# Kernel optimization log

Hardware: AMD Instinct MI355X
Metric: run time of the kernel (lower is better)

## Reference

```python
import jax, jax.numpy as jnp
import numpy as np

K = 2            # negative:positive edge ratio (init arg k)
N_NODES = 4096
N_EDGES = 8192
FEAT = 64


def setup_inputs() -> dict:
    key = jax.random.key(0)
    k1, k2, k3 = jax.random.split(key, 3)
    node_feature = jax.random.normal(k1, (N_NODES, FEAT), dtype=jnp.float32)
    edge_src = jax.random.randint(k2, (N_EDGES,), 0, N_NODES, dtype=jnp.int32)
    edge_dst = jax.random.randint(k3, (N_EDGES,), 0, N_NODES, dtype=jnp.int32)
    return {"node_feature": node_feature, "edge_src": edge_src, "edge_dst": edge_dst}


def reference(node_feature, edge_src, edge_dst):
    E = edge_src.shape[0]
    N = node_feature.shape[0]
    # [E, E] pairwise mask: candidate column j is valid for row i iff
    # dst[j] != dst[i] and dst[j] != src[i]
    valid = (edge_dst[:, None] != edge_dst[None, :]) & (edge_src[:, None] != edge_dst[None, :])
    # unsorted_segment_min over rows grouped by edge_src -> [N, E]
    segmin = jax.ops.segment_min(valid.astype(jnp.int8), edge_src, num_segments=N)
    # gather back per edge -> [E, E], flatten
    m = segmin[edge_src].reshape(-1).astype(bool)  # [E*E]
    num_negatives = jnp.sum(m)
    ratio = num_negatives // E                      # integer ratio as in TF code
    keep_prob = (K / ratio).astype(jnp.float32)
    u = jax.random.uniform(jax.random.key(42), (E * E,), dtype=jnp.float32)
    keep = m & (u < keep_prob)
    # fixed-size (jit-friendly) stand-in for tf.boolean_mask: expected count is K*E;
    # pad/truncate to exactly K*E kept flat indices (fill_value=0 pads).
    idx = jnp.nonzero(keep, size=K * E, fill_value=0)[0]
    rows = idx // E
    cols = idx % E
    edge_src_neg = edge_src[rows]
    edge_dst_neg = edge_dst[cols]
    return edge_src_neg, edge_dst_neg
```

## Files before the change

kernel.cpp:

```cpp
#include <hip/hip_runtime.h>
#include <stdint.h>
#include <math.h>

typedef unsigned int u32;
typedef unsigned long long u64;

#define E_CNT   8192
#define N_CNT   4096
#define TOT_N   (1u << 26)
#define OUT_K   16384
#define NODE_BM_WORDS 128
#define N_CHUNKS 1024

#define OFF_BAD      0x000000
#define OFF_CNT_DST  0x200000
#define OFF_CNT_SRC  0x204000
#define OFF_CCOUNT   0x208000
#define OFF_SCALARS  0x209000
#define OFF_KEEPBM   0x210000
#define ZERO_BYTES   0x209040

__device__ __forceinline__ u32 rotl32(u32 x, u32 d) {
  return __builtin_amdgcn_alignbit(x, x, 32u - d);
}

__device__ __forceinline__ void threefry_0_42(u32 x0, u32 x1, u32& o0, u32& o1) {
  const u32 k0 = 0u, k1 = 42u, k2 = 0x1BD11BF0u;
  x0 += k0; x1 += k1;
#define TF_R(r) { x0 += x1; x1 = rotl32(x1, r); x1 ^= x0; }
  TF_R(13) TF_R(15) TF_R(26) TF_R(6)
  x0 += k1; x1 += k2 + 1u;
  TF_R(17) TF_R(29) TF_R(16) TF_R(24)
  x0 += k2; x1 += k0 + 2u;
  TF_R(13) TF_R(15) TF_R(26) TF_R(6)
  x0 += k0; x1 += k1 + 3u;
  TF_R(17) TF_R(29) TF_R(16) TF_R(24)
  x0 += k1; x1 += k2 + 4u;
  TF_R(13) TF_R(15) TF_R(26) TF_R(6)
  x0 += k2; x1 += k0 + 5u;
#undef TF_R
  o0 = x0; o1 = x1;
}

__global__ void k_build(const int* __restrict__ src, const int* __restrict__ dst,
                        u32* __restrict__ bad, u32* __restrict__ cnt_dst,
                        u32* __restrict__ cnt_src, int* __restrict__ out) {
  int tid = blockIdx.x * 256 + threadIdx.x;
  if (tid < N_CNT) {
    atomicOr(&bad[(u32)tid * NODE_BM_WORDS + ((u32)tid >> 5)], 1u << (tid & 31));
  }
  u32 s = (u32)src[tid], d = (u32)dst[tid];
  atomicOr(&bad[s * NODE_BM_WORDS + (d >> 5)], 1u << (d & 31));
  atomicAdd(&cnt_dst[d], 1u);
  atomicAdd(&cnt_src[s], 1u);
  int s0 = src[0], d0 = dst[0];
  out[tid] = s0;            out[tid + E_CNT] = s0;
  out[OUT_K + tid] = d0;    out[OUT_K + tid + E_CNT] = d0;
}

__global__ void __launch_bounds__(1024) k_rowcount(const u32* __restrict__ bad,
                                                   const u32* __restrict__ cnt_dst,
                                                   const u32* __restrict__ cnt_src,
                                                   u32* __restrict__ scal) {
  int wv = threadIdx.x >> 6, ln = threadIdx.x & 63;
  int n = blockIdx.x * 16 + wv;
  const u32* row = bad + (u32)n * NODE_BM_WORDS;
  u32 sum = 0;
#pragma unroll
  for (int h = 0; h < 2; ++h) {
    int w = ln + h * 64;
    u32 bits = row[w];
    while (bits) { int b = __ffs(bits) - 1; sum += cnt_dst[(w << 5) + b]; bits &= bits - 1; }
  }
#pragma unroll
  for (int off = 32; off > 0; off >>= 1) sum += __shfl_down(sum, off, 64);
  __shared__ u32 part[16];
  if (ln == 0) part[wv] = ((u32)E_CNT - sum) * cnt_src[n];
  __syncthreads();
  if (threadIdx.x == 0) {
    u32 tot = 0;
#pragma unroll
    for (int k = 0; k < 16; ++k) tot += part[k];
    atomicAdd(&scal[0], tot);
    __threadfence();
    if (atomicAdd(&scal[1], 1u) == 255u) {
      u32 nn = atomicAdd(&scal[0], 0u);
      u32 ratio = nn >> 13;
      float kp = 2.0f / (float)ratio;
      u32 T = (u32)ceil((double)kp * 8388608.0);
      atomicExch(&scal[2], T);
    }
  }
}

__global__ void __launch_bounds__(256) k_sample(const int* __restrict__ src,
                                                const int* __restrict__ dst,
                                                const u32* __restrict__ bad,
                                                const u32* __restrict__ scal,
                                                u64* __restrict__ keep_bm,
                                                u32* __restrict__ ccount) {
  u32 base = blockIdx.x * 1024u;
  u32 wv = threadIdx.x >> 6, ln = threadIdx.x & 63;
  u32 i0 = base + wv * 256u + ln;
  u32 T = scal[2];
  u64 words[4];
#pragma unroll
  for (int k = 0; k < 4; ++k) {
    u32 i = i0 + (u32)k * 64u;
    u32 o0, o1;
    threefry_0_42(0u, i, o0, o1);
    bool keep = ((o0 ^ o1) >> 9) < T;
    if (keep) {
      u32 n = (u32)src[i >> 13]; u32 v = (u32)dst[i & 8191];
      keep = ((bad[n * NODE_BM_WORDS + (v >> 5)] >> (v & 31)) & 1u) == 0u;
    }
    words[k] = __ballot(keep);
  }
  if (ln == 0) {
    u32 widx = (base >> 6) + wv * 4u;
    ulonglong2* p = (ulonglong2*)&keep_bm[widx];
    p[0] = make_ulonglong2(words[0], words[1]);
    p[1] = make_ulonglong2(words[2], words[3]);
    u32 c = (u32)__popcll(words[0]) + (u32)__popcll(words[1]) +
            (u32)__popcll(words[2]) + (u32)__popcll(words[3]);
    if (c) atomicAdd(&ccount[base >> 16], c);
  }
}

__global__ void k_compact(const int* __restrict__ src, const int* __restrict__ dst,
                          const u64* __restrict__ keep_bm, const u32* __restrict__ ccount,
                          int* __restrict__ out) {
  int c = blockIdx.x;
  int t = threadIdx.x;
  __shared__ u32 s[256];
  __shared__ u32 base_sh;

  u32 v[4]; u32 sum4 = 0;
#pragma unroll
  for (int k = 0; k < 4; ++k) { v[k] = ccount[4 * t + k]; sum4 += v[k]; }
  s[t] = sum4; __syncthreads();
  for (int off = 1; off < 256; off <<= 1) {
    u32 x = (t >= off) ? s[t - off] : 0u;
    __syncthreads();
    s[t] += x;
    __syncthreads();
  }
  if (t == (c >> 2)) {
    u32 excl = s[t] - sum4;
#pragma unroll
    for (int k = 0; k < 4; ++k) if (k < (c & 3)) excl += v[k];
    base_sh = excl;
  }
  __syncthreads();
  u32 coff_c = base_sh;
  __syncthreads();

  const u64* words = keep_bm + (size_t)c * 1024;
  u64 w[4];
  u32 cnt = 0;
#pragma unroll
  for (int k = 0; k < 4; ++k) { w[k] = words[4 * t + k]; cnt += (u32)__popcll(w[k]); }
  s[t] = cnt; __syncthreads();
  for (int off = 1; off < 256; off <<= 1) {
    u32 x = (t >= off) ? s[t - off] : 0u;
    __syncthreads();
    s[t] += x;
    __syncthreads();
  }
  u32 rank = coff_c + s[t] - cnt;
  u32 tbase = (u32)c * 65536u + (u32)t * 256u;
#pragma unroll
  for (int k = 0; k < 4; ++k) {
    u64 bits = w[k];
    while (bits) {
      int b = __ffsll((unsigned long long)bits) - 1;
      if (rank < OUT_K) {
        u32 tt = tbase + (u32)k * 64u + (u32)b;
        out[rank]         = src[tt >> 13];
        out[OUT_K + rank] = dst[tt & 8191];
      }
      rank++;
      bits &= bits - 1;
    }
  }
}

extern "C" void kernel_launch(void* const* d_in, const int* in_sizes, int n_in,
                              void* d_out, int out_size, void* d_ws, size_t ws_size,
                              hipStream_t stream) {
  const int* src = (const int*)d_in[1];
  const int* dst = (const int*)d_in[2];
  int* out = (int*)d_out;
  char* ws = (char*)d_ws;

  u32* bad     = (u32*)(ws + OFF_BAD);
  u32* cnt_dst = (u32*)(ws + OFF_CNT_DST);
  u32* cnt_src = (u32*)(ws + OFF_CNT_SRC);
  u32* ccount  = (u32*)(ws + OFF_CCOUNT);
  u32* scal    = (u32*)(ws + OFF_SCALARS);
  u64* keep_bm = (u64*)(ws + OFF_KEEPBM);

  hipMemsetAsync(ws, 0, ZERO_BYTES, stream);
  k_build<<<E_CNT / 256, 256, 0, stream>>>(src, dst, bad, cnt_dst, cnt_src, out);
  k_rowcount<<<N_CNT / 16, 1024, 0, stream>>>(bad, cnt_dst, cnt_src, scal);
  k_sample<<<TOT_N / 1024, 256, 0, stream>>>(src, dst, bad, scal, keep_bm, ccount);
  k_compact<<<N_CHUNKS, 256, 0, stream>>>(src, dst, keep_bm, ccount, out);
}
```

Measured before the change: 192.0 us.

## Interleave two threefry streams per thread and defer mask lookups past RNG ballot

The sampling kernel now computes two interleaved threefry hashes per thread, doubling per-thread work and halving the grid. Known-zero key additions are dropped. The threshold is pre-shifted so the comparison uses the raw xor bits. Bitmap lookups are deferred until after an RNG-only ballot and skipped for wave words with no candidates. This targets ALU latency and divergent gather cost in the dominant kernel, at the cost of higher register pressure and fewer blocks.

```diff
diff --git a/kernel.cpp b/kernel.cpp
--- a/kernel.cpp
+++ b/kernel.cpp
@@ -24,22 +24,27 @@
   return __builtin_amdgcn_alignbit(x, x, 32u - d);
 }
 
-__device__ __forceinline__ void threefry_0_42(u32 x0, u32 x1, u32& o0, u32& o1) {
-  const u32 k0 = 0u, k1 = 42u, k2 = 0x1BD11BF0u;
-  x0 += k0; x1 += k1;
-#define TF_R(r) { x0 += x1; x1 = rotl32(x1, r); x1 ^= x0; }
-  TF_R(13) TF_R(15) TF_R(26) TF_R(6)
-  x0 += k1; x1 += k2 + 1u;
-  TF_R(17) TF_R(29) TF_R(16) TF_R(24)
-  x0 += k2; x1 += k0 + 2u;
-  TF_R(13) TF_R(15) TF_R(26) TF_R(6)
-  x0 += k0; x1 += k1 + 3u;
-  TF_R(17) TF_R(29) TF_R(16) TF_R(24)
-  x0 += k1; x1 += k2 + 4u;
-  TF_R(13) TF_R(15) TF_R(26) TF_R(6)
-  x0 += k2; x1 += k0 + 5u;
-#undef TF_R
-  o0 = x0; o1 = x1;
+__device__ __forceinline__ void threefry2_0_42(u32 ia, u32 ib, u32& bits_a, u32& bits_b) {
+  const u32 k1 = 42u, k2 = 0x1BD11BF0u;
+  u32 a0 = ia + k1, a1r;
+  u32 b0 = ib + k1;
+  u32 A0 = 0u, A1 = a0;
+  u32 B0 = 0u, B1 = b0;
+#define R2(r) { A0 += A1; B0 += B1; A1 = rotl32(A1, r); B1 = rotl32(B1, r); A1 ^= A0; B1 ^= B0; }
+  R2(13) R2(15) R2(26) R2(6)
+  A0 += k1; B0 += k1; A1 += k2 + 1u; B1 += k2 + 1u;
+  R2(17) R2(29) R2(16) R2(24)
+  A0 += k2; B0 += k2; A1 += 2u; B1 += 2u;
+  R2(13) R2(15) R2(26) R2(6)
+   A1 += k1 + 3u; B1 += k1 + 3u;
+  R2(17) R2(29) R2(16) R2(24)
+  A0 += k1; B0 += k1; A1 += k2 + 4u; B1 += k2 + 4u;
+  R2(13) R2(15) R2(26) R2(6)
+  A0 += k2; B0 += k2; A1 += 5u; B1 += 5u;
+#undef R2
+  bits_a = A0 ^ A1;
+  bits_b = B0 ^ B1;
+  (void)a1r;
 }
 
 __global__ void k_build(const int* __restrict__ src, const int* __restrict__ dst,
@@ -88,7 +93,8 @@
       u32 ratio = nn >> 13;
       float kp = 2.0f / (float)ratio;
       u32 T = (u32)ceil((double)kp * 8388608.0);
-      atomicExch(&scal[2], T);
+      u32 T9 = (T >= (1u << 23)) ? 0xFFFFFFFFu : (T << 9);
+      atomicExch(&scal[2], T9);
     }
   }
 }
@@ -99,31 +105,46 @@
                                                 const u32* __restrict__ scal,
                                                 u64* __restrict__ keep_bm,
                                                 u32* __restrict__ ccount) {
-  u32 base = blockIdx.x * 1024u;
   u32 wv = threadIdx.x >> 6, ln = threadIdx.x & 63;
-  u32 i0 = base + wv * 256u + ln;
-  u32 T = scal[2];
-  u64 words[4];
-#pragma unroll
-  for (int k = 0; k < 4; ++k) {
-    u32 i = i0 + (u32)k * 64u;
-    u32 o0, o1;
-    threefry_0_42(0u, i, o0, o1);
-    bool keep = ((o0 ^ o1) >> 9) < T;
-    if (keep) {
-      u32 n = (u32)src[i >> 13]; u32 v = (u32)dst[i & 8191];
-      keep = ((bad[n * NODE_BM_WORDS + (v >> 5)] >> (v & 31)) & 1u) == 0u;
+  u32 i0w = blockIdx.x * 2048u + wv * 512u;
+  u32 T9 = scal[2];
+  u64 words[8];
+  u64 any = 0;
+#pragma unroll
+  for (int j = 0; j < 4; ++j) {
+    u32 ia = i0w + (u32)j * 128u + ln;
+    u32 ba, bb;
+    threefry2_0_42(ia, ia + 64u, ba, bb);
+    u64 ma = __ballot(ba < T9);
+    u64 mb = __ballot(bb < T9);
+    words[2 * j] = ma; words[2 * j + 1] = mb;
+    any |= ma | mb;
+  }
+  if (any) {
+#pragma unroll
+    for (int k = 0; k < 8; ++k) {
+      if (words[k]) {
+        u32 i = i0w + (u32)k * 64u + ln;
+        bool kp = (words[k] >> ln) & 1ull;
+        if (kp) {
+          u32 n = (u32)src[i >> 13]; u32 v = (u32)dst[i & 8191];
+          kp = ((bad[n * NODE_BM_WORDS + (v >> 5)] >> (v & 31)) & 1u) == 0u;
+        }
+        words[k] = __ballot(kp);
+      }
     }
-    words[k] = __ballot(keep);
   }
   if (ln == 0) {
-    u32 widx = (base >> 6) + wv * 4u;
+    u32 widx = i0w >> 6;
     ulonglong2* p = (ulonglong2*)&keep_bm[widx];
     p[0] = make_ulonglong2(words[0], words[1]);
     p[1] = make_ulonglong2(words[2], words[3]);
-    u32 c = (u32)__popcll(words[0]) + (u32)__popcll(words[1]) +
-            (u32)__popcll(words[2]) + (u32)__popcll(words[3]);
-    if (c) atomicAdd(&ccount[base >> 16], c);
+    p[2] = make_ulonglong2(words[4], words[5]);
+    p[3] = make_ulonglong2(words[6], words[7]);
+    u32 c = 0;
+#pragma unroll
+    for (int k = 0; k < 8; ++k) c += (u32)__popcll(words[k]);
+    if (c) atomicAdd(&ccount[i0w >> 16], c);
   }
 }
 
@@ -203,6 +224,6 @@
   hipMemsetAsync(ws, 0, ZERO_BYTES, stream);
   k_build<<<E_CNT / 256, 256, 0, stream>>>(src, dst, bad, cnt_dst, cnt_src, out);
   k_rowcount<<<N_CNT / 16, 1024, 0, stream>>>(bad, cnt_dst, cnt_src, scal);
-  k_sample<<<TOT_N / 1024, 256, 0, stream>>>(src, dst, bad, scal, keep_bm, ccount);
+  k_sample<<<TOT_N / 2048, 256, 0, stream>>>(src, dst, bad, scal, keep_bm, ccount);
   k_compact<<<N_CHUNKS, 256, 0, stream>>>(src, dst, keep_bm, ccount, out);
 }
```

Result: no change. 189.1 us (-1.5%).
